# Performance work log

Hardware: AMD Instinct MI355X
Metric: run time of the kernel (lower is better)

## Reference

```python
import jax, jax.numpy as jnp
import numpy as np

GAM1 = 1.0
GAM2 = 1.0
EPS = 0.01


def setup_inputs() -> dict:
    key = jax.random.key(0)
    k1, k2 = jax.random.split(key)
    m, p, k = 262144, 128, 10
    x = jax.random.normal(k1, (m, p), dtype=jnp.float32)
    y = jax.random.randint(k2, (m,), 0, k, dtype=jnp.int32)
    return {"x": x, "y": y, "num_classes": k}


def reference(x, y, num_classes):
    m, p = x.shape
    I = jnp.eye(p, dtype=x.dtype)
    scalar = p / (m * EPS)

    # W = x.T, so W @ W.T == x.T @ x  (p x p Gram)
    cov = x.T @ x
    discrimn_empi = jnp.linalg.slogdet(I + GAM1 * scalar * cov)[1] / 2.0
    discrimn_theo = jnp.linalg.slogdet(I + scalar * cov)[1] / 2.0

    # per-class compress loss: logdet(I + p/(n_j*eps) * W_j W_j^T) * n_j / m
    onehot = jax.nn.one_hot(y, num_classes, dtype=x.dtype)  # [m, k]
    counts = onehot.sum(axis=0)                             # [k]

    def class_cov(col):  # col: [m] 0/1 mask for one class
        return (x * col[:, None]).T @ x  # [p, p]

    covs = jax.lax.map(class_cov, onehot.T)  # [k, p, p], sequential over k classes

    safe_counts = jnp.maximum(counts, 1.0)
    scal = p / (safe_counts * EPS)                              # [k]
    lds = jnp.linalg.slogdet(I[None] + scal[:, None, None] * covs)[1]  # [k]
    compress = jnp.sum(jnp.where(counts > 0, lds * counts / m, 0.0)) / 2.0

    total_loss_empi = GAM2 * (-discrimn_empi) + compress
    return total_loss_empi, discrimn_empi, discrimn_theo, compress
```

## Files before the change

kernel.cpp:

```cpp
#include <hip/hip_runtime.h>

#define K 10
#define P 128
#define EPSV 0.01f
#define GAM1 1.0f
#define GAM2 1.0f
#define CH 512
#define SK 64
#define KS 68
#define SORTCH 2048
#define NTHR 256

typedef __attribute__((ext_vector_type(8))) short bf16x8;
typedef __attribute__((ext_vector_type(4))) short s16x4;
typedef __attribute__((ext_vector_type(4))) float f32x4;

static __device__ __forceinline__ short f2bf(float f) {
    unsigned u = __float_as_uint(f);
    u = (u + 0x7FFFu + ((u >> 16) & 1u)) >> 16;
    return (short)u;
}

__global__ void hist_kernel(const int* __restrict__ y, int* __restrict__ blk_counts, int m) {
    __shared__ int h[K];
    int t = threadIdx.x;
    if (t < K) h[t] = 0;
    __syncthreads();
    int base = blockIdx.x * SORTCH;
    int rows = min(SORTCH, m - base);
    for (int i = t; i < rows; i += NTHR) atomicAdd(&h[y[base + i]], 1);
    __syncthreads();
    if (t < K) blk_counts[blockIdx.x * K + t] = h[t];
}

__global__ void scan_kernel(const int* __restrict__ blk_counts, int* __restrict__ blk_offsets,
                            int* __restrict__ counts, int* __restrict__ pstart, int nb) {
    __shared__ int s[K][128];
    __shared__ int sps[K + 1];
    int t = threadIdx.x;
    int own[K];
    if (t < 128) {
        for (int c = 0; c < K; ++c) {
            int v = (t < nb) ? blk_counts[t * K + c] : 0;
            own[c] = v;
            s[c][t] = v;
        }
    }
    __syncthreads();
    for (int off = 1; off < 128; off <<= 1) {
        int tmp[K];
        if (t < 128)
            for (int c = 0; c < K; ++c) tmp[c] = (t >= off) ? s[c][t - off] : 0;
        __syncthreads();
        if (t < 128)
            for (int c = 0; c < K; ++c) s[c][t] += tmp[c];
        __syncthreads();
    }
    if (t == 0) {
        int run = 0;
        for (int c = 0; c < K; ++c) {
            sps[c] = run;
            int tot = s[c][127];
            counts[c] = tot;
            pstart[c] = run;
            run += ((tot + CH - 1) / CH) * CH;
        }
        sps[K] = run;
        pstart[K] = run;
    }
    __syncthreads();
    if (t < nb)
        for (int c = 0; c < K; ++c)
            blk_offsets[t * K + c] = sps[c] + s[c][t] - own[c];
}

__global__ void scatter_kernel(const int* __restrict__ y, const int* __restrict__ blk_offsets,
                               int* __restrict__ perm, int m) {
    __shared__ int cur[K];
    int t = threadIdx.x;
    if (t < K) cur[t] = blk_offsets[blockIdx.x * K + t];
    __syncthreads();
    int base = blockIdx.x * SORTCH;
    int rows = min(SORTCH, m - base);
    for (int i = t; i < rows; i += NTHR) {
        int row = base + i;
        int pos = atomicAdd(&cur[y[row]], 1);
        perm[pos] = row;
    }
}

__global__ __launch_bounds__(NTHR) void gram_kernel(const float* __restrict__ x,
                                                    const int* __restrict__ perm,
                                                    const int* __restrict__ pstart,
                                                    float* __restrict__ grams) {
    __shared__ int pm[CH];
    __shared__ short xsT[P * KS];
    int t = threadIdx.x;
    long base = (long)blockIdx.x * CH;
    int cls = 0;
    for (int c = 1; c < K; ++c)
        if (base >= (long)pstart[c]) cls = c;
    for (int i = t; i < CH; i += NTHR) pm[i] = perm[base + i];

    const int lane = t & 63;
    const int wave = t >> 6;
    const int m16 = lane & 15;
    const int quad = lane >> 4;
    const int wr = wave >> 1;
    const int wc = wave & 1;
    const int c2 = t & 63;
    const int rg = t >> 6;

    f32x4 acc[4][4];
#pragma unroll
    for (int a = 0; a < 4; ++a)
#pragma unroll
        for (int b = 0; b < 4; ++b) acc[a][b] = (f32x4){0.f, 0.f, 0.f, 0.f};

    __syncthreads();

    for (int s = 0; s < CH / SK; ++s) {
        int sb = s * SK;
        float2 v[16];
#pragma unroll
        for (int ii = 0; ii < 16; ++ii) {
            int r = pm[sb + rg * 16 + ii];
            if (r >= 0) v[ii] = ((const float2*)(x + (size_t)r * P))[c2];
            else { v[ii].x = 0.f; v[ii].y = 0.f; }
        }
        __syncthreads();
        short b0[16], b1[16];
#pragma unroll
        for (int ii = 0; ii < 16; ++ii) { b0[ii] = f2bf(v[ii].x); b1[ii] = f2bf(v[ii].y); }
        int col0 = 2 * c2, col1 = 2 * c2 + 1;
#pragma unroll
        for (int q = 0; q < 4; ++q) {
            s16x4 w0 = {b0[q * 4], b0[q * 4 + 1], b0[q * 4 + 2], b0[q * 4 + 3]};
            s16x4 w1 = {b1[q * 4], b1[q * 4 + 1], b1[q * 4 + 2], b1[q * 4 + 3]};
            *(s16x4*)&xsT[col0 * KS + rg * 16 + q * 4] = w0;
            *(s16x4*)&xsT[col1 * KS + rg * 16 + q * 4] = w1;
        }
        __syncthreads();
#pragma unroll
        for (int kk = 0; kk < 2; ++kk) {
            int k0 = kk * 32 + quad * 8;
            bf16x8 af[4], bfr[4];
#pragma unroll
            for (int a = 0; a < 4; ++a) {
                int colA = wr * 64 + a * 16 + m16;
                union { bf16x8 v8; s16x4 h[2]; } u;
                u.h[0] = *(s16x4*)&xsT[colA * KS + k0];
                u.h[1] = *(s16x4*)&xsT[colA * KS + k0 + 4];
                af[a] = u.v8;
            }
#pragma unroll
            for (int b = 0; b < 4; ++b) {
                int colB = wc * 64 + b * 16 + m16;
                union { bf16x8 v8; s16x4 h[2]; } u;
                u.h[0] = *(s16x4*)&xsT[colB * KS + k0];
                u.h[1] = *(s16x4*)&xsT[colB * KS + k0 + 4];
                bfr[b] = u.v8;
            }
#pragma unroll
            for (int a = 0; a < 4; ++a)
#pragma unroll
                for (int b = 0; b < 4; ++b)
                    acc[a][b] = __builtin_amdgcn_mfma_f32_16x16x32_bf16(af[a], bfr[b], acc[a][b], 0, 0, 0);
        }
    }
    float* g = grams + (size_t)cls * P * P;
#pragma unroll
    for (int a = 0; a < 4; ++a)
#pragma unroll
        for (int b = 0; b < 4; ++b)
#pragma unroll
            for (int r = 0; r < 4; ++r) {
                int gi = wr * 64 + a * 16 + quad * 4 + r;
                int gj = wc * 64 + b * 16 + m16;
                if (gi <= gj) atomicAdd(&g[gi * P + gj], acc[a][b][r]);
            }
}

__global__ __launch_bounds__(1024) void logdet_kernel(const float* __restrict__ grams,
                                                      const int* __restrict__ counts,
                                                      float* __restrict__ logd, int m) {
    __shared__ float A[P * P];
    int t = threadIdx.x, b = blockIdx.x;
    float scale;
    if (b == 0) scale = GAM1 * (float)P / ((float)m * EPSV);
    else if (b == 1) scale = (float)P / ((float)m * EPSV);
    else {
        float cnt = (float)counts[b - 2];
        if (cnt < 1.f) cnt = 1.f;
        scale = (float)P / (cnt * EPSV);
    }
    for (int idx = t; idx < P * P; idx += 1024) {
        int i = idx >> 7, c = idx & (P - 1);
        int src = (i <= c) ? (i * P + c) : (c * P + i);
        float sgm;
        if (b < 2) {
            float ssum = 0.f;
            for (int cc = 0; cc < K; ++cc) ssum += grams[cc * P * P + src];
            sgm = ssum;
        } else {
            sgm = grams[(b - 2) * P * P + src];
        }
        A[idx] = scale * sgm + ((i == c) ? 1.f : 0.f);
    }
    __syncthreads();

    const int cq = t & 31;
    const int rg = t >> 5;
    const int c0 = cq * 4;
    for (int j = 0; j < P - 1; ++j) {
        float inv = 1.0f / A[j * P + j];
        if (c0 + 3 > j) {
            f32x4 ajc = *(f32x4*)&A[j * P + c0];
            if (c0 + 0 <= j) ajc[0] = 0.f;
            if (c0 + 1 <= j) ajc[1] = 0.f;
            if (c0 + 2 <= j) ajc[2] = 0.f;
            for (int i = j + 1 + rg; i < P; i += 32) {
                float lij = A[i * P + j] * inv;
                f32x4 vv = *(f32x4*)&A[i * P + c0];
                vv[0] -= lij * ajc[0];
                vv[1] -= lij * ajc[1];
                vv[2] -= lij * ajc[2];
                vv[3] -= lij * ajc[3];
                *(f32x4*)&A[i * P + c0] = vv;
            }
        }
        __syncthreads();
    }
    if (t < P) atomicAdd(&logd[b], logf(A[t * P + t]));
}

__global__ void final_kernel(const float* __restrict__ logd, const int* __restrict__ counts,
                             float* __restrict__ out, int m) {
    if (threadIdx.x == 0 && blockIdx.x == 0) {
        float empi = 0.5f * logd[0];
        float theo = 0.5f * logd[1];
        float comp = 0.f;
        for (int c = 0; c < K; ++c) {
            float cnt = (float)counts[c];
            if (cnt > 0.f) comp += logd[2 + c] * cnt / (float)m;
        }
        comp *= 0.5f;
        out[0] = GAM2 * (-empi) + comp;
        out[1] = empi;
        out[2] = theo;
        out[3] = comp;
    }
}

extern "C" void kernel_launch(void* const* d_in, const int* in_sizes, int n_in,
                              void* d_out, int out_size, void* d_ws, size_t ws_size,
                              hipStream_t stream) {
    const float* x = (const float*)d_in[0];
    const int* y = (const int*)d_in[1];
    int m = in_sizes[1];
    int nbs = (m + SORTCH - 1) / SORTCH;
    int nbg = (m + CH - 1) / CH + K;

    char* ws = (char*)d_ws;
    float* grams = (float*)ws;
    float* logd = (float*)(ws + 655360);
    int* counts = (int*)(ws + 655424);
    int* pstart = (int*)(ws + 655488);
    int* blk_counts = (int*)(ws + 655616);
    int* blk_offsets = (int*)(ws + 655616 + (size_t)nbs * K * 4);
    int* perm = (int*)(ws + 655616 + 2 * (size_t)nbs * K * 4);

    hipMemsetAsync(ws, 0, 655488, stream);
    hipMemsetAsync(perm, 0xFF, (size_t)nbg * CH * 4, stream);

    hist_kernel<<<nbs, NTHR, 0, stream>>>(y, blk_counts, m);
    scan_kernel<<<1, NTHR, 0, stream>>>(blk_counts, blk_offsets, counts, pstart, nbs);
    scatter_kernel<<<nbs, NTHR, 0, stream>>>(y, blk_offsets, perm, m);
    gram_kernel<<<nbg, NTHR, 0, stream>>>(x, perm, pstart, grams);
    logdet_kernel<<<K + 2, 1024, 0, stream>>>(grams, counts, logd, m);
    final_kernel<<<1, 1, 0, stream>>>(logd, counts, (float*)d_out, m);
}
```

Measured before the change: 350.4 us.

## Replace unblocked Gaussian elimination with blocked LU in logdet kernel

The logdet kernel's 127-step unblocked elimination, with a block barrier after every pivot, becomes a blocked factorization with 32-wide panels. One wavefront factors each diagonal panel in registers using shuffles and solves the U row strip. All 256 threads then apply a rank-32 trailing update in 4x4 register tiles. This cuts barriers from about 127 to about 8 and raises arithmetic intensity on LDS, at the cost of serial single-wave panel work and a smaller block (256 threads) with heavy register use.

```diff
diff --git a/kernel.cpp b/kernel.cpp
--- a/kernel.cpp
+++ b/kernel.cpp
@@ -181,9 +181,9 @@
             }
 }
 
-__global__ __launch_bounds__(1024) void logdet_kernel(const float* __restrict__ grams,
-                                                      const int* __restrict__ counts,
-                                                      float* __restrict__ logd, int m) {
+__global__ __launch_bounds__(256) void logdet_kernel(const float* __restrict__ grams,
+                                                     const int* __restrict__ counts,
+                                                     float* __restrict__ logd, int m) {
     __shared__ float A[P * P];
     int t = threadIdx.x, b = blockIdx.x;
     float scale;
@@ -194,7 +194,7 @@
         if (cnt < 1.f) cnt = 1.f;
         scale = (float)P / (cnt * EPSV);
     }
-    for (int idx = t; idx < P * P; idx += 1024) {
+    for (int idx = t; idx < P * P; idx += 256) {
         int i = idx >> 7, c = idx & (P - 1);
         int src = (i <= c) ? (i * P + c) : (c * P + i);
         float sgm;
@@ -209,29 +209,98 @@
     }
     __syncthreads();
 
-    const int cq = t & 31;
-    const int rg = t >> 5;
-    const int c0 = cq * 4;
-    for (int j = 0; j < P - 1; ++j) {
-        float inv = 1.0f / A[j * P + j];
-        if (c0 + 3 > j) {
-            f32x4 ajc = *(f32x4*)&A[j * P + c0];
-            if (c0 + 0 <= j) ajc[0] = 0.f;
-            if (c0 + 1 <= j) ajc[1] = 0.f;
-            if (c0 + 2 <= j) ajc[2] = 0.f;
-            for (int i = j + 1 + rg; i < P; i += 32) {
-                float lij = A[i * P + j] * inv;
-                f32x4 vv = *(f32x4*)&A[i * P + c0];
-                vv[0] -= lij * ajc[0];
-                vv[1] -= lij * ajc[1];
-                vv[2] -= lij * ajc[2];
-                vv[3] -= lij * ajc[3];
-                *(f32x4*)&A[i * P + c0] = vv;
-            }
-        }
-        __syncthreads();
-    }
-    if (t < P) atomicAdd(&logd[b], logf(A[t * P + t]));
+    const int lane = t & 63;
+    const int wid = t >> 6;
+    float lsum = 0.f;
+
+    for (int bs = 0; bs < 4; ++bs) {
+        const int j0 = bs * 32;
+        if (wid == 0) {
+            float a[32];
+            if (lane < 32) {
+#pragma unroll
+                for (int cc = 0; cc < 8; ++cc)
+                    *(f32x4*)&a[cc * 4] = *(f32x4*)&A[(j0 + lane) * P + j0 + cc * 4];
+            } else {
+#pragma unroll
+                for (int cc = 0; cc < 32; ++cc) a[cc] = 0.f;
+            }
+            float myinv = 0.f;
+#pragma unroll
+            for (int tt = 0; tt < 32; ++tt) {
+                float utt = __shfl(a[tt], tt);
+                float inv = __builtin_amdgcn_rcpf(utt);
+                lsum += __logf(utt);
+                if (lane == tt) myinv = inv;
+                bool act = (lane < 32) && (lane > tt);
+                float lm = act ? a[tt] * inv : 0.f;
+                if (act) a[tt] = lm;
+#pragma unroll
+                for (int k2 = tt + 1; k2 < 32; ++k2) {
+                    float utk = __shfl(a[k2], tt);
+                    a[k2] -= lm * utk;
+                }
+            }
+            if (lane < 32) A[(j0 + lane) * P + j0 + lane] = myinv;
+
+            if (bs < 3) {
+                int nc = P - j0 - 32;
+                int c0 = j0 + 32 + lane;
+                int c1 = c0 + 64;
+                bool v0 = lane < nc;
+                bool v1 = lane + 64 < nc;
+                int c0a = v0 ? c0 : (j0 + 32);
+                int c1a = v1 ? c1 : (j0 + 32);
+                float ua[32], ub[32];
+#pragma unroll
+                for (int j = 0; j < 32; ++j) {
+                    float s0 = A[(j0 + j) * P + c0a];
+                    float s1 = A[(j0 + j) * P + c1a];
+#pragma unroll
+                    for (int t2 = 0; t2 < j; ++t2) {
+                        float ljt = __shfl(a[t2], j);
+                        s0 -= ljt * ua[t2];
+                        s1 -= ljt * ub[t2];
+                    }
+                    ua[j] = s0; ub[j] = s1;
+                    if (v0) A[(j0 + j) * P + c0] = s0;
+                    if (v1) A[(j0 + j) * P + c1] = s1;
+                }
+            }
+        }
+        __syncthreads();
+
+        if (bs < 3) {
+            int nc = P - j0 - 32;
+            int nt = nc >> 2;
+            int ntiles = nt * nt;
+            for (int tile = t; tile < ntiles; tile += 256) {
+                int ti = tile / nt, tk = tile - ti * nt;
+                int i0 = j0 + 32 + ti * 4, k0 = j0 + 32 + tk * 4;
+                f32x4 acc0 = {0, 0, 0, 0}, acc1 = {0, 0, 0, 0};
+                f32x4 acc2 = {0, 0, 0, 0}, acc3 = {0, 0, 0, 0};
+#pragma unroll
+                for (int j = 0; j < 32; ++j) {
+                    const float* row = &A[(j0 + j) * P];
+                    float invd = row[j0 + j];
+                    f32x4 ui = *(const f32x4*)&row[i0];
+                    f32x4 uk = *(const f32x4*)&row[k0];
+                    uk *= invd;
+                    acc0 += ui[0] * uk;
+                    acc1 += ui[1] * uk;
+                    acc2 += ui[2] * uk;
+                    acc3 += ui[3] * uk;
+                }
+                f32x4* r0 = (f32x4*)&A[(i0 + 0) * P + k0];
+                f32x4* r1 = (f32x4*)&A[(i0 + 1) * P + k0];
+                f32x4* r2 = (f32x4*)&A[(i0 + 2) * P + k0];
+                f32x4* r3 = (f32x4*)&A[(i0 + 3) * P + k0];
+                *r0 -= acc0; *r1 -= acc1; *r2 -= acc2; *r3 -= acc3;
+            }
+            __syncthreads();
+        }
+    }
+    if (t == 0) logd[b] = lsum;
 }
 
 __global__ void final_kernel(const float* __restrict__ logd, const int* __restrict__ counts,
@@ -277,6 +346,6 @@
     scan_kernel<<<1, NTHR, 0, stream>>>(blk_counts, blk_offsets, counts, pstart, nbs);
     scatter_kernel<<<nbs, NTHR, 0, stream>>>(y, blk_offsets, perm, m);
     gram_kernel<<<nbg, NTHR, 0, stream>>>(x, perm, pstart, grams);
-    logdet_kernel<<<K + 2, 1024, 0, stream>>>(grams, counts, logd, m);
+    logdet_kernel<<<K + 2, 256, 0, stream>>>(grams, counts, logd, m);
     final_kernel<<<1, 1, 0, stream>>>(logd, counts, (float*)d_out, m);
 }
```

Measured after the change: 355.1 us. No clear change (+1.3%).
